# Kernel tuning notes

Hardware: AMD Instinct MI355X
Metric: run time of the kernel (lower is better)

## Reference

```python
import jax, jax.numpy as jnp
import numpy as np

B, N_NODES, T_IN = 512, 32, 12
HID, HEADS, OUT_CH, DEG = 64, 8, 9, 8


def setup_inputs() -> dict:
    key = jax.random.key(0)
    ks = jax.random.split(key, 26)
    rn = lambda k, s, sc=0.1: (jax.random.normal(k, s, jnp.float32) * sc)
    E = B * N_NODES * DEG
    src = jax.random.randint(ks[0], (E,), 0, N_NODES, jnp.int32)
    dst = jax.random.randint(ks[1], (E,), 0, N_NODES, jnp.int32)
    off = jnp.repeat(jnp.arange(B, dtype=jnp.int32) * N_NODES, N_NODES * DEG)
    edge_index = jnp.stack([src + off, dst + off])  # block-diagonal batched graph
    x = jax.random.normal(ks[2], (B, N_NODES, T_IN), jnp.float32)
    return {
        "x": x,
        "edge_index": edge_index,
        # gat1: in=T_IN -> HEADS*HID, concat
        "W1": rn(ks[3], (T_IN, HEADS * HID)),
        "a_src1": rn(ks[4], (HEADS, HID)),
        "a_dst1": rn(ks[5], (HEADS, HID)),
        "b1": rn(ks[6], (HEADS * HID,), 0.01),
        # gat2: in=HEADS*HID -> HID, heads=1, mean (concat=False)
        "W2": rn(ks[7], (HEADS * HID, HID), 0.05),
        "a_src2": rn(ks[8], (1, HID)),
        "a_dst2": rn(ks[9], (1, HID)),
        "b2": rn(ks[10], (HID,), 0.01),
        "gamma": jnp.ones((HID,), jnp.float32),
        "beta": jnp.zeros((HID,), jnp.float32),
        # gru1: input_size=N_NODES(=32), hidden=HID
        "Wi1": rn(ks[11], (3 * HID, N_NODES)),
        "Wh1": rn(ks[12], (3 * HID, HID)),
        "bi1": rn(ks[13], (3 * HID,), 0.01),
        "bh1": rn(ks[14], (3 * HID,), 0.01),
        # gru2: input_size=HID, hidden=HID
        "Wi2": rn(ks[15], (3 * HID, HID)),
        "Wh2": rn(ks[16], (3 * HID, HID)),
        "bi2": rn(ks[17], (3 * HID,), 0.01),
        "bh2": rn(ks[18], (3 * HID,), 0.01),
        "Wf": rn(ks[19], (OUT_CH, HID)),
        "bf": rn(ks[20], (OUT_CH,), 0.01),
    }


def _gat_layer(x, src, dst, W, a_s, a_d, b, concat):
    # PyG GATConv (eval mode, self-loops already appended by caller)
    Nn = x.shape[0]
    heads, hc = a_s.shape
    h = (x @ W).reshape(Nn, heads, hc)                 # [N, H, C]
    es = jnp.sum(h * a_s, axis=-1)                     # [N, H]
    ed = jnp.sum(h * a_d, axis=-1)
    e = jax.nn.leaky_relu(es[src] + ed[dst], 0.2)      # [E, H]
    m = jax.ops.segment_max(e, dst, num_segments=Nn)
    p = jnp.exp(e - m[dst])
    s = jax.ops.segment_sum(p, dst, num_segments=Nn)
    alpha = p / (s[dst] + 1e-16)                       # per-dst softmax
    out = jax.ops.segment_sum(h[src] * alpha[:, :, None], dst, num_segments=Nn)
    out = out.reshape(Nn, heads * hc) if concat else out.mean(axis=1)
    return out + b


def _gru(x, Wi, Wh, bi, bh):
    # torch.nn.GRU (batch_first) single layer; x: [B, T, F]
    H = Wh.shape[1]
    xi = x @ Wi.T + bi                                 # [B, T, 3H]
    def step(h, xt):
        gh = h @ Wh.T + bh
        r = jax.nn.sigmoid(xt[:, :H] + gh[:, :H])
        z = jax.nn.sigmoid(xt[:, H:2 * H] + gh[:, H:2 * H])
        n = jnp.tanh(xt[:, 2 * H:] + r * gh[:, 2 * H:])
        hn = (1.0 - z) * n + z * h
        return hn, hn
    h0 = jnp.zeros((x.shape[0], H), x.dtype)
    _, ys = jax.lax.scan(step, h0, jnp.swapaxes(xi, 0, 1))
    return jnp.swapaxes(ys, 0, 1)


def reference(x, edge_index, W1, a_src1, a_dst1, b1, W2, a_src2, a_dst2, b2,
              gamma, beta, Wi1, Wh1, bi1, bh1, Wi2, Wh2, bi2, bh2, Wf, bf):
    Bsz, Nn_, T = x.shape
    Nn = Bsz * Nn_
    xf = x.reshape(Nn, T)                              # dropout is identity in eval
    sl = jnp.arange(Nn, dtype=edge_index.dtype)        # PyG add_self_loops=True
    src = jnp.concatenate([edge_index[0], sl])
    dst = jnp.concatenate([edge_index[1], sl])
    h = jax.nn.elu(_gat_layer(xf, src, dst, W1, a_src1, a_dst1, b1, True))
    h = jax.nn.elu(_gat_layer(h, src, dst, W2, a_src2, a_dst2, b2, False))
    mu = h.mean(-1, keepdims=True)
    var = ((h - mu) ** 2).mean(-1, keepdims=True)
    h = (h - mu) / jnp.sqrt(var + 1e-5) * gamma + beta
    seq = h.reshape(Bsz, Nn_, -1).transpose(0, 2, 1)   # [B, HID(seq), N_NODES(feat)]
    g = _gru(seq, Wi1, Wh1, bi1, bh1)
    g = _gru(g, Wi2, Wh2, bi2, bh2)
    return g[:, -1, :] @ Wf.T + bf                     # [B, OUT_CH]
```

## Files before the change

kernel.cpp:

```cpp
#include <hip/hip_runtime.h>
#include <hip/hip_bf16.h>
#include <stdint.h>

#define BATCH 512
#define NN 32
#define T_IN 12
#define HID 64
#define HEADS 8
#define OUT_CH 9
#define EPB (NN*8)
#define ETOT (EPB+NN)
#define F1 (HEADS*HID)

using u16 = unsigned short;
using u32 = unsigned int;
typedef _Float16 f16;
typedef _Float16 f16x2 __attribute__((ext_vector_type(2)));
typedef u32 v4u __attribute__((ext_vector_type(4)));

__device__ __forceinline__ float bf2f(u16 u){ return __uint_as_float(((u32)u)<<16); }
__device__ __forceinline__ u16 f2bf(float f){
    u32 x = __float_as_uint(f);
    u32 r = (x + 0x7FFFu + ((x>>16)&1u))>>16;
    return (u16)r;
}
__device__ __forceinline__ u32 packf16(float a, float b){
    f16x2 p; p.x=(f16)a; p.y=(f16)b; return __builtin_bit_cast(u32,p);
}
__device__ __forceinline__ u16 f2h16(float a){ f16 h=(f16)a; return __builtin_bit_cast(u16,h); }
__device__ __forceinline__ float h16f(u16 v){ f16 h=__builtin_bit_cast(f16,v); return (float)h; }
__device__ __forceinline__ float lof(u32 w){ return (float)__builtin_bit_cast(f16x2,w).x; }
__device__ __forceinline__ float hif(u32 w){ return (float)__builtin_bit_cast(f16x2,w).y; }
__device__ __forceinline__ float dot2(u32 a, u32 b, float c){
#if __has_builtin(__builtin_amdgcn_fdot2)
    return __builtin_amdgcn_fdot2(__builtin_bit_cast(f16x2,a), __builtin_bit_cast(f16x2,b), c, false);
#else
    return fmaf(lof(a),lof(b), fmaf(hif(a),hif(b), c));
#endif
}
__device__ __forceinline__ float elu1(float x){ return x > 0.f ? x : (__expf(x)-1.f); }
__device__ __forceinline__ float sigm(float x){ return 1.f/(1.f+__expf(-x)); }
__device__ __forceinline__ float tanh_(float x){ return 1.f - 2.f/(__expf(2.f*x)+1.f); }
__device__ __forceinline__ u32 fenc(float v){
    u32 b=__float_as_uint(v);
    return (b&0x80000000u) ? ~b : (b|0x80000000u);
}
__device__ __forceinline__ float fdec(u32 k){
    return __uint_as_float((k&0x80000000u) ? (k&0x7FFFFFFFu) : ~k);
}

#define DOT4(acc,A,W) do{ acc=dot2(A.x,W.x,acc); acc=dot2(A.y,W.y,acc); \
                          acc=dot2(A.z,W.z,acc); acc=dot2(A.w,W.w,acc); }while(0)
#define DOT32(acc,A0,A1,A2,A3,A4,A5,A6,A7,W0,W1,W2,W3,W4,W5,W6,W7) do{ \
    DOT4(acc,A0,W0); DOT4(acc,A1,W1); DOT4(acc,A2,W2); DOT4(acc,A3,W3); \
    DOT4(acc,A4,W4); DOT4(acc,A5,W5); DOT4(acc,A6,W6); DOT4(acc,A7,W7); }while(0)

__global__ __launch_bounds__(256) void k_detect(const u32* __restrict__ xw, int* __restrict__ flag){
    __shared__ int cnt;
    if(threadIdx.x==0) cnt=0;
    __syncthreads();
    int c=0;
    for(int i=threadIdx.x;i<4096;i+=256){
        u32 w=xw[i];
        if(w & 0x7FFFFFFFu){
            u32 el=(w>>7)&0xFFu;
            if(el>=0x90u) c++;
        }
    }
    atomicAdd(&cnt,c);
    __syncthreads();
    if(threadIdx.x==0) *flag = (cnt>256) ? 1 : 0;
}

struct CvtDesc {
    const void* src[16];
    void*       dst[16];
    int         n[16];
};

__global__ __launch_bounds__(256) void k_convert(CvtDesc d, const int* __restrict__ flag){
    const int seg = blockIdx.x;
    const int f = *flag;
    const void* s = d.src[seg];
    const int n = d.n[seg];
    const int stride = gridDim.y*256;
    float* o=(float*)d.dst[seg];
    for(int i=blockIdx.y*256+threadIdx.x;i<n;i+=stride)
        o[i] = f ? ((const float*)s)[i] : bf2f(((const u16*)s)[i]);
}

__global__ __launch_bounds__(256) void k_prep(
    const void* __restrict__ W2src, u16* __restrict__ W2i,
    const void* __restrict__ Wi1, const void* __restrict__ Wh1,
    const void* __restrict__ Wi2, const void* __restrict__ Wh2,
    u32* __restrict__ wpk, const int* __restrict__ flag)
{
    const int f=*flag;
    if(blockIdx.x<128){
        int i = blockIdx.x*256+threadIdx.x;
        int k=i>>6, j=i&63;
        float v = f? ((const float*)W2src)[i] : bf2f(((const u16*)W2src)[i]);
        W2i[ (((size_t)(k>>3)*64 + j)<<3) + (k&7) ] = f2h16(v);
    } else {
        int w = (blockIdx.x-128)*256+threadIdx.x;
        int m = w/6144;
        int rem = w - m*6144;
        int row = rem>>5, kw = rem&31;
        const void* s = (m==0)?Wi1 : (m==1)?Wh1 : (m==2)?Wi2 : Wh2;
        int K = (m==0)?32:64;
        int k0=2*kw, k1=k0+1;
        float v0=0.f, v1=0.f;
        if(k0<K) v0 = f? ((const float*)s)[row*K+k0] : bf2f(((const u16*)s)[row*K+k0]);
        if(k1<K) v1 = f? ((const float*)s)[row*K+k1] : bf2f(((const u16*)s)[row*K+k1]);
        wpk[w]=packf16(v0,v1);
    }
}

__global__ __launch_bounds__(256,2) void k_gat1(
    const float* __restrict__ x, const int* __restrict__ ei,
    const float* __restrict__ W1, const float* __restrict__ a_s, const float* __restrict__ a_d,
    const float* __restrict__ b1, u32* __restrict__ h1g)
{
    const int b = blockIdx.x, t = threadIdx.x;
    __shared__ __align__(16) float s_x[NN][12];
    __shared__ float s_W1[T_IN*F1];
    __shared__ __align__(16) u16 s_h[NN][520];
    __shared__ __align__(16) u32 s_aspk[HEADS*32], s_adpk[HEADS*32];
    __shared__ float s_es[NN][HEADS], s_ed[NN][HEADS];
    __shared__ unsigned char s_src[ETOT], s_dst[ETOT];
    __shared__ float s_al[ETOT][HEADS];
    __shared__ u32 s_mx[NN*HEADS];
    __shared__ float s_sm[NN*HEADS], s_inv[NN*HEADS];
    __shared__ int s_cnt[NN], s_off[NN], s_fil[NN];
    __shared__ short s_lst[ETOT];

    for(int i=t;i<NN*T_IN;i+=256) s_x[i/12][i%12] = x[b*NN*T_IN + i];
    for(int i=t;i<T_IN*F1;i+=256) s_W1[i]=W1[i];
    s_aspk[t]=packf16(a_s[2*t],a_s[2*t+1]);
    s_adpk[t]=packf16(a_d[2*t],a_d[2*t+1]);
    s_mx[t]=0u; s_sm[t]=0.f;
    if(t<EPB){
        s_src[t] = (unsigned char)(ei[b*EPB+t] - b*NN);
        s_dst[t] = (unsigned char)(ei[(size_t)BATCH*EPB + b*EPB+t] - b*NN);
    }
    if(t<NN){ s_src[EPB+t]=s_dst[EPB+t]=(unsigned char)t; s_cnt[t]=0; s_fil[t]=0; }
    __syncthreads();

    {
        float w0[12], w1[12];
        #pragma unroll
        for(int k=0;k<12;k++){ w0[k]=s_W1[k*F1+t]; w1[k]=s_W1[k*F1+t+256]; }
        for(int n=0;n<NN;n++){
            const float4* xp=(const float4*)s_x[n];
            float4 xa=xp[0], xb=xp[1], xc=xp[2];
            float A=0.f,B=0.f;
            A=fmaf(xa.x,w0[0],A); A=fmaf(xa.y,w0[1],A); A=fmaf(xa.z,w0[2],A); A=fmaf(xa.w,w0[3],A);
            A=fmaf(xb.x,w0[4],A); A=fmaf(xb.y,w0[5],A); A=fmaf(xb.z,w0[6],A); A=fmaf(xb.w,w0[7],A);
            A=fmaf(xc.x,w0[8],A); A=fmaf(xc.y,w0[9],A); A=fmaf(xc.z,w0[10],A); A=fmaf(xc.w,w0[11],A);
            B=fmaf(xa.x,w1[0],B); B=fmaf(xa.y,w1[1],B); B=fmaf(xa.z,w1[2],B); B=fmaf(xa.w,w1[3],B);
            B=fmaf(xb.x,w1[4],B); B=fmaf(xb.y,w1[5],B); B=fmaf(xb.z,w1[6],B); B=fmaf(xb.w,w1[7],B);
            B=fmaf(xc.x,w1[8],B); B=fmaf(xc.y,w1[9],B); B=fmaf(xc.z,w1[10],B); B=fmaf(xc.w,w1[11],B);
            s_h[n][t]=f2h16(A); s_h[n][t+256]=f2h16(B);
        }
    }
    for(int e=t;e<ETOT;e+=256) atomicAdd(&s_cnt[s_dst[e]],1);
    __syncthreads();

    {
        int n=t&31, hd=t>>5;
        const v4u* hp=(const v4u*)((const u16*)s_h[n] + hd*64);
        v4u h0=hp[0],h1=hp[1],h2=hp[2],h3=hp[3],h4=hp[4],h5=hp[5],h6=hp[6],h7=hp[7];
        const v4u* ap=(const v4u*)&s_aspk[hd*32];
        const v4u* dp=(const v4u*)&s_adpk[hd*32];
        float e1=0.f,e2=0.f;
        { v4u w=ap[0]; DOT4(e1,h0,w); w=ap[1]; DOT4(e1,h1,w); w=ap[2]; DOT4(e1,h2,w); w=ap[3]; DOT4(e1,h3,w);
          w=ap[4]; DOT4(e1,h4,w); w=ap[5]; DOT4(e1,h5,w); w=ap[6]; DOT4(e1,h6,w); w=ap[7]; DOT4(e1,h7,w); }
        { v4u w=dp[0]; DOT4(e2,h0,w); w=dp[1]; DOT4(e2,h1,w); w=dp[2]; DOT4(e2,h2,w); w=dp[3]; DOT4(e2,h3,w);
          w=dp[4]; DOT4(e2,h4,w); w=dp[5]; DOT4(e2,h5,w); w=dp[6]; DOT4(e2,h6,w); w=dp[7]; DOT4(e2,h7,w); }
        s_es[n][hd]=e1; s_ed[n][hd]=e2;
    }
    if(t==0){ int o=0; for(int i=0;i<NN;i++){ s_off[i]=o; o+=s_cnt[i]; } }
    __syncthreads();

    for(int e=t;e<ETOT;e+=256){
        int d=s_dst[e]; int p=atomicAdd(&s_fil[d],1); s_lst[s_off[d]+p]=(short)e;
    }
    for(int i=t;i<ETOT*HEADS;i+=256){
        int e=i>>3, hd=i&7;
        int sr=s_src[e], d=s_dst[e];
        float v = s_es[sr][hd]+s_ed[d][hd];
        v = v>0.f? v : 0.2f*v;
        s_al[e][hd]=v;
        atomicMax(&s_mx[d*8+hd], fenc(v));
    }
    __syncthreads();

    for(int i=t;i<ETOT*HEADS;i+=256){
        int e=i>>3, hd=i&7;
        int d=s_dst[e];
        float p=__expf(s_al[e][hd]-fdec(s_mx[d*8+hd]));
        s_al[e][hd]=p;
        atomicAdd(&s_sm[d*8+hd], p);
    }
    __syncthreads();
    s_inv[t]=1.f/(s_sm[t]+1e-16f);
    __syncthreads();

    {
        int d=t&31, hd=t>>5;
        int o=s_off[d], cnt=s_cnt[d];
        float inv=s_inv[d*8+hd];
        size_t obase = ((size_t)(b*NN+d))*256 + hd*32;
        #pragma unroll
        for(int ch=0;ch<2;ch++){
            float acc[32];
            #pragma unroll
            for(int i=0;i<32;i++) acc[i]=0.f;
            for(int i=0;i<cnt;i++){
                int e=s_lst[o+i]; float a=s_al[e][hd]; int sr=s_src[e];
                const v4u* hp=(const v4u*)((const u16*)s_h[sr] + hd*64 + ch*32);
                v4u p0=hp[0],p1=hp[1],p2=hp[2],p3=hp[3];
                #define ACC2(i,w) acc[2*(i)]+=a*lof(w); acc[2*(i)+1]+=a*hif(w);
                ACC2(0,p0.x) ACC2(1,p0.y) ACC2(2,p0.z) ACC2(3,p0.w)
                ACC2(4,p1.x) ACC2(5,p1.y) ACC2(6,p1.z) ACC2(7,p1.w)
                ACC2(8,p2.x) ACC2(9,p2.y) ACC2(10,p2.z) ACC2(11,p2.w)
                ACC2(12,p3.x) ACC2(13,p3.y) ACC2(14,p3.z) ACC2(15,p3.w)
                #undef ACC2
            }
            u32* op = h1g + obase + ch*16;
            #pragma unroll
            for(int j=0;j<16;j++){
                float v0=elu1(acc[2*j]*inv   + b1[hd*64+ch*32+2*j]);
                float v1=elu1(acc[2*j+1]*inv + b1[hd*64+ch*32+2*j+1]);
                op[j]=packf16(v0,v1);
            }
        }
    }
}

__global__ __launch_bounds__(256,2) void k_gat2ln(
    const u32* __restrict__ h1g, const int* __restrict__ ei,
    const uint4* __restrict__ W2i, const float* __restrict__ a_s2, const float* __restrict__ a_d2,
    const float* __restrict__ b2, const float* __restrict__ gam, const float* __restrict__ bet,
    float* __restrict__ hlng)
{
    const int b=blockIdx.x, t=threadIdx.x;
    __shared__ __align__(16) u32 s_h1[NN*260];
    __shared__ float s_h2[NN][HID];
    __shared__ float s_es[NN], s_ed[NN];
    __shared__ unsigned char s_src[ETOT], s_dst[ETOT];
    __shared__ float s_al[ETOT];
    __shared__ u32 s_mx[NN];
    __shared__ float s_sm[NN], s_inv[NN];
    __shared__ int s_cnt[NN], s_off[NN], s_fil[NN];
    __shared__ short s_lst[ETOT];

    { const u32* g = h1g + (size_t)b*8192;
      for(int w=t; w<8192; w+=256){ int n=w>>8, c=w&255; s_h1[n*260+c]=g[w]; } }
    if(t<EPB){
        s_src[t]=(unsigned char)(ei[b*EPB+t]-b*NN);
        s_dst[t]=(unsigned char)(ei[(size_t)BATCH*EPB+b*EPB+t]-b*NN);
    }
    if(t<NN){ s_src[EPB+t]=s_dst[EPB+t]=(unsigned char)t;
              s_cnt[t]=0; s_fil[t]=0; s_mx[t]=0u; s_sm[t]=0.f; }
    __syncthreads();

    for(int e=t;e<ETOT;e+=256) atomicAdd(&s_cnt[s_dst[e]],1);
    {
        int n0=(t>>5)<<2, j0=(t&31)<<1;
        const u32* r0=&s_h1[(n0+0)*260];
        const u32* r1=&s_h1[(n0+1)*260];
        const u32* r2=&s_h1[(n0+2)*260];
        const u32* r3=&s_h1[(n0+3)*260];
        float a00=0,a01=0,a10=0,a11=0,a20=0,a21=0,a30=0,a31=0;
        for(int kb=0;kb<64;kb++){
            uint4 A0=*(const uint4*)&r0[kb*4];
            uint4 A1=*(const uint4*)&r1[kb*4];
            uint4 A2=*(const uint4*)&r2[kb*4];
            uint4 A3=*(const uint4*)&r3[kb*4];
            const uint4* wp=&W2i[kb*64+j0];
            uint4 w0=wp[0], w1=wp[1];
            a00=dot2(A0.x,w0.x,a00); a00=dot2(A0.y,w0.y,a00); a00=dot2(A0.z,w0.z,a00); a00=dot2(A0.w,w0.w,a00);
            a01=dot2(A0.x,w1.x,a01); a01=dot2(A0.y,w1.y,a01); a01=dot2(A0.z,w1.z,a01); a01=dot2(A0.w,w1.w,a01);
            a10=dot2(A1.x,w0.x,a10); a10=dot2(A1.y,w0.y,a10); a10=dot2(A1.z,w0.z,a10); a10=dot2(A1.w,w0.w,a10);
            a11=dot2(A1.x,w1.x,a11); a11=dot2(A1.y,w1.y,a11); a11=dot2(A1.z,w1.z,a11); a11=dot2(A1.w,w1.w,a11);
            a20=dot2(A2.x,w0.x,a20); a20=dot2(A2.y,w0.y,a20); a20=dot2(A2.z,w0.z,a20); a20=dot2(A2.w,w0.w,a20);
            a21=dot2(A2.x,w1.x,a21); a21=dot2(A2.y,w1.y,a21); a21=dot2(A2.z,w1.z,a21); a21=dot2(A2.w,w1.w,a21);
            a30=dot2(A3.x,w0.x,a30); a30=dot2(A3.y,w0.y,a30); a30=dot2(A3.z,w0.z,a30); a30=dot2(A3.w,w0.w,a30);
            a31=dot2(A3.x,w1.x,a31); a31=dot2(A3.y,w1.y,a31); a31=dot2(A3.z,w1.z,a31); a31=dot2(A3.w,w1.w,a31);
        }
        s_h2[n0+0][j0]=a00; s_h2[n0+0][j0+1]=a01;
        s_h2[n0+1][j0]=a10; s_h2[n0+1][j0+1]=a11;
        s_h2[n0+2][j0]=a20; s_h2[n0+2][j0+1]=a21;
        s_h2[n0+3][j0]=a30; s_h2[n0+3][j0+1]=a31;
    }
    __syncthreads();

    {
        int n=t>>3, g=t&7;
        float e1=0,e2=0;
        #pragma unroll
        for(int cc=0; cc<8; cc++){
            float hv = s_h2[n][g*8+cc];
            e1 += hv*a_s2[g*8+cc];
            e2 += hv*a_d2[g*8+cc];
        }
        #pragma unroll
        for(int m=1;m<8;m<<=1){ e1 += __shfl_xor(e1,m,64); e2 += __shfl_xor(e2,m,64); }
        if(g==0){ s_es[n]=e1; s_ed[n]=e2; }
    }
    if(t==0){ int o=0; for(int i=0;i<NN;i++){ s_off[i]=o; o+=s_cnt[i]; } }
    __syncthreads();

    for(int e=t;e<ETOT;e+=256){
        int d=s_dst[e]; int p=atomicAdd(&s_fil[d],1); s_lst[s_off[d]+p]=(short)e;
    }
    for(int e=t;e<ETOT;e+=256){
        int d=s_dst[e];
        float v = s_es[s_src[e]] + s_ed[d];
        v = v>0.f? v:0.2f*v;
        s_al[e]=v;
        atomicMax(&s_mx[d], fenc(v));
    }
    __syncthreads();

    for(int e=t;e<ETOT;e+=256){
        int d=s_dst[e];
        float p=__expf(s_al[e]-fdec(s_mx[d]));
        s_al[e]=p;
        atomicAdd(&s_sm[d], p);
    }
    __syncthreads();
    if(t<NN) s_inv[t]=1.f/(s_sm[t]+1e-16f);
    __syncthreads();

    {
        int n=t>>3, g=t&7;
        float acc[8];
        #pragma unroll
        for(int i=0;i<8;i++) acc[i]=0;
        int o=s_off[n], cnt=s_cnt[n];
        float inv=s_inv[n];
        for(int i=0;i<cnt;i++){
            int e=s_lst[o+i]; float a=s_al[e]; int sr=s_src[e];
            const float4* hp=(const float4*)&s_h2[sr][g*8];
            float4 v0=hp[0], v1=hp[1];
            acc[0]+=a*v0.x; acc[1]+=a*v0.y; acc[2]+=a*v0.z; acc[3]+=a*v0.w;
            acc[4]+=a*v1.x; acc[5]+=a*v1.y; acc[6]+=a*v1.z; acc[7]+=a*v1.w;
        }
        float sum=0,sq=0;
        #pragma unroll
        for(int i=0;i<8;i++){
            float v = elu1(acc[i]*inv + b2[g*8+i]);
            acc[i]=v; sum+=v; sq+=v*v;
        }
        #pragma unroll
        for(int m=1;m<8;m<<=1){ sum+=__shfl_xor(sum,m,64); sq+=__shfl_xor(sq,m,64); }
        float mu = sum*(1.f/64.f);
        float var = sq*(1.f/64.f) - mu*mu;
        float rs = rsqrtf(var + 1e-5f);
        float* outp = hlng + (size_t)b*HID*NN;
        #pragma unroll
        for(int i=0;i<8;i++){
            int c=g*8+i;
            float v=(acc[i]-mu)*rs*gam[c] + bet[c];
            outp[c*NN + n] = v;
        }
    }
}

__global__ __launch_bounds__(256,2) void k_grum(
    const float* __restrict__ hlng, const u32* __restrict__ wpk,
    const float* __restrict__ bi1, const float* __restrict__ bh1,
    const float* __restrict__ bi2, const float* __restrict__ bh2,
    const float* __restrict__ Wf, const float* __restrict__ bfv,
    void* __restrict__ outp, const int* __restrict__ flag)
{
    const int b=blockIdx.x, t=threadIdx.x;
    const int wave=t>>6, u=t&63;
    __shared__ __align__(16) u32 s_x[64*16];
    __shared__ __align__(16) u32 s_xi[64*96];
    __shared__ __align__(16) u32 s_y[64*32];
    __shared__ __align__(16) u32 s_h[32];
    __shared__ float s_hf[64];

    { const float2* g=(const float2*)(hlng + (size_t)b*2048);
      for(int w=t;w<1024;w+=256){ float2 f=g[w]; s_x[w]=packf16(f.x,f.y); } }
    __syncthreads();

    if(t<192){
        const v4u* wr=(const v4u*)wpk + t*8;
        v4u w0=wr[0],w1=wr[1],w2=wr[2],w3=wr[3];
        float bias=bi1[t];
        u16* o=(u16*)s_xi + t;
        for(int step=0;step<64;step++){
            const v4u* xp=(const v4u*)&s_x[step*16];
            v4u a0=xp[0],a1=xp[1],a2=xp[2],a3=xp[3];
            float a=bias;
            DOT4(a,a0,w0); DOT4(a,a1,w1); DOT4(a,a2,w2); DOT4(a,a3,w3);
            o[step*192]=f2h16(a);
        }
    }
    __syncthreads();

    if(wave==0){
        const v4u* wh=(const v4u*)(wpk + 6144);
        v4u r0=wh[u*8+0],r1=wh[u*8+1],r2=wh[u*8+2],r3=wh[u*8+3],
            r4=wh[u*8+4],r5=wh[u*8+5],r6=wh[u*8+6],r7=wh[u*8+7];
        v4u z0=wh[(64+u)*8+0],z1=wh[(64+u)*8+1],z2=wh[(64+u)*8+2],z3=wh[(64+u)*8+3],
            z4=wh[(64+u)*8+4],z5=wh[(64+u)*8+5],z6=wh[(64+u)*8+6],z7=wh[(64+u)*8+7];
        v4u n0=wh[(128+u)*8+0],n1=wh[(128+u)*8+1],n2=wh[(128+u)*8+2],n3=wh[(128+u)*8+3],
            n4=wh[(128+u)*8+4],n5=wh[(128+u)*8+5],n6=wh[(128+u)*8+6],n7=wh[(128+u)*8+7];
        float bhr=bh1[u], bhz=bh1[64+u], bhn=bh1[128+u];
        if(u<32) s_h[u]=0u;
        float h=0.f;
        for(int st=0;st<64;st++){
            const u16* xr=(const u16*)s_xi + st*192;
            float xir=h16f(xr[u]), xiz=h16f(xr[64+u]), xin=h16f(xr[128+u]);
            const v4u* hp=(const v4u*)s_h;
            v4u A0=hp[0],A1=hp[1],A2=hp[2],A3=hp[3],A4=hp[4],A5=hp[5],A6=hp[6],A7=hp[7];
            float gr=bhr,gz=bhz,gn=bhn;
            DOT32(gr,A0,A1,A2,A3,A4,A5,A6,A7,r0,r1,r2,r3,r4,r5,r6,r7);
            DOT32(gz,A0,A1,A2,A3,A4,A5,A6,A7,z0,z1,z2,z3,z4,z5,z6,z7);
            DOT32(gn,A0,A1,A2,A3,A4,A5,A6,A7,n0,n1,n2,n3,n4,n5,n6,n7);
            float rr=sigm(xir+gr), zz=sigm(xiz+gz);
            float nn=tanh_(xin + rr*gn);
            h=(1.f-zz)*nn+zz*h;
            u16 hv=f2h16(h);
            ((u16*)s_h)[u]=hv;
            ((u16*)s_y)[st*64+u]=hv;
        }
    }
    __syncthreads();

    if(t<192){
        const v4u* wr=(const v4u*)(wpk + 2*6144) + t*8;
        v4u w0=wr[0],w1=wr[1],w2=wr[2],w3=wr[3],w4=wr[4],w5=wr[5],w6=wr[6],w7=wr[7];
        float bias=bi2[t];
        u16* o=(u16*)s_xi + t;
        for(int step=0;step<64;step++){
            const v4u* xp=(const v4u*)&s_y[step*32];
            v4u a0=xp[0],a1=xp[1],a2=xp[2],a3=xp[3],a4=xp[4],a5=xp[5],a6=xp[6],a7=xp[7];
            float a=bias;
            DOT32(a,a0,a1,a2,a3,a4,a5,a6,a7,w0,w1,w2,w3,w4,w5,w6,w7);
            o[step*192]=f2h16(a);
        }
    }
    __syncthreads();

    if(wave==0){
        const v4u* wh=(const v4u*)(wpk + 3*6144);
        v4u r0=wh[u*8+0],r1=wh[u*8+1],r2=wh[u*8+2],r3=wh[u*8+3],
            r4=wh[u*8+4],r5=wh[u*8+5],r6=wh[u*8+6],r7=wh[u*8+7];
        v4u z0=wh[(64+u)*8+0],z1=wh[(64+u)*8+1],z2=wh[(64+u)*8+2],z3=wh[(64+u)*8+3],
            z4=wh[(64+u)*8+4],z5=wh[(64+u)*8+5],z6=wh[(64+u)*8+6],z7=wh[(64+u)*8+7];
        v4u n0=wh[(128+u)*8+0],n1=wh[(128+u)*8+1],n2=wh[(128+u)*8+2],n3=wh[(128+u)*8+3],
            n4=wh[(128+u)*8+4],n5=wh[(128+u)*8+5],n6=wh[(128+u)*8+6],n7=wh[(128+u)*8+7];
        float bhr=bh2[u], bhz=bh2[64+u], bhn=bh2[128+u];
        if(u<32) s_h[u]=0u;
        float h=0.f;
        for(int st=0;st<64;st++){
            const u16* xr=(const u16*)s_xi + st*192;
            float xir=h16f(xr[u]), xiz=h16f(xr[64+u]), xin=h16f(xr[128+u]);
            const v4u* hp=(const v4u*)s_h;
            v4u A0=hp[0],A1=hp[1],A2=hp[2],A3=hp[3],A4=hp[4],A5=hp[5],A6=hp[6],A7=hp[7];
            float gr=bhr,gz=bhz,gn=bhn;
            DOT32(gr,A0,A1,A2,A3,A4,A5,A6,A7,r0,r1,r2,r3,r4,r5,r6,r7);
            DOT32(gz,A0,A1,A2,A3,A4,A5,A6,A7,z0,z1,z2,z3,z4,z5,z6,z7);
            DOT32(gn,A0,A1,A2,A3,A4,A5,A6,A7,n0,n1,n2,n3,n4,n5,n6,n7);
            float rr=sigm(xir+gr), zz=sigm(xiz+gz);
            float nn=tanh_(xin + rr*gn);
            h=(1.f-zz)*nn+zz*h;
            ((u16*)s_h)[u]=f2h16(h);
        }
        s_hf[u]=h;
    }
    __syncthreads();

    if(t<OUT_CH){
        float acc=bfv[t];
        const float4* wp=(const float4*)(Wf + t*64);
        const float4* hp=(const float4*)s_hf;
        #pragma unroll
        for(int k=0;k<16;k++){
            float4 w=wp[k], v=hp[k];
            acc += w.x*v.x + w.y*v.y + w.z*v.z + w.w*v.w;
        }
        if(*flag) ((float*)outp)[b*OUT_CH+t]=acc;
        else      ((u16*)outp)[b*OUT_CH+t]=f2bf(acc);
    }
}

extern "C" void kernel_launch(void* const* d_in, const int* in_sizes, int n_in,
                              void* d_out, int out_size, void* d_ws, size_t ws_size,
                              hipStream_t stream)
{
    char* ws=(char*)d_ws;
    int* flag = (int*)ws;
    float* cf = (float*)(ws + 256);
    float* c_x   = cf; cf+=196608;
    float* c_W1  = cf; cf+=6144;
    float* c_as1 = cf; cf+=512;
    float* c_ad1 = cf; cf+=512;
    float* c_b1  = cf; cf+=512;
    float* c_as2 = cf; cf+=64;
    float* c_ad2 = cf; cf+=64;
    float* c_b2  = cf; cf+=64;
    float* c_gam = cf; cf+=64;
    float* c_bet = cf; cf+=64;
    float* c_bi1 = cf; cf+=192;
    float* c_bh1 = cf; cf+=192;
    float* c_bi2 = cf; cf+=192;
    float* c_bh2 = cf; cf+=192;
    float* c_Wf  = cf; cf+=576;
    float* c_bf  = cf; cf+=9;
    uintptr_t p = ((uintptr_t)cf + 255) & ~(uintptr_t)255;
    u16* c_W2i = (u16*)p;
    p = (p + 32768*2 + 255) & ~(uintptr_t)255;
    u32* wpk = (u32*)p;
    p = (p + 24576*4 + 255) & ~(uintptr_t)255;
    u32* h1g = (u32*)p;
    p = (p + (size_t)BATCH*NN*256*4 + 255) & ~(uintptr_t)255;
    float* hlng = (float*)p;

    const int* ei = (const int*)d_in[1];

    CvtDesc d;
    const int srcIdx[16] = {0,2,3,4,5,7,8,9,10,11,14,15,18,19,20,21};
    void* dsts[16] = {c_x,c_W1,c_as1,c_ad1,c_b1,c_as2,c_ad2,c_b2,c_gam,c_bet,
                      c_bi1,c_bh1,c_bi2,c_bh2,c_Wf,c_bf};
    const int ns[16] = {196608,6144,512,512,512,64,64,64,64,64,
                        192,192,192,192,576,9};
    for(int i=0;i<16;i++){ d.src[i]=d_in[srcIdx[i]]; d.dst[i]=dsts[i]; d.n[i]=ns[i]; }

    k_detect <<<dim3(1),dim3(256),0,stream>>>((const u32*)d_in[0], flag);
    k_convert<<<dim3(16,8),dim3(256),0,stream>>>(d, flag);
    k_prep   <<<dim3(224),dim3(256),0,stream>>>(d_in[6], c_W2i,
                                                d_in[12], d_in[13], d_in[16], d_in[17], wpk, flag);
    k_gat1   <<<dim3(BATCH),dim3(256),0,stream>>>(c_x,ei,c_W1,c_as1,c_ad1,c_b1,h1g);
    k_gat2ln <<<dim3(BATCH),dim3(256),0,stream>>>(h1g,ei,(const uint4*)c_W2i,c_as2,c_ad2,c_b2,c_gam,c_bet,hlng);
    k_grum   <<<dim3(BATCH),dim3(256),0,stream>>>(hlng, wpk, c_bi1,c_bh1,c_bi2,c_bh2,
                                                  c_Wf, c_bf, d_out, flag);
}
```

Baseline: 260.1 us.

## Process two batches per GRU block and transpose GAT attention layout

```diff
diff --git a/kernel.cpp b/kernel.cpp
--- a/kernel.cpp
+++ b/kernel.cpp
@@ -17,6 +17,7 @@
 typedef _Float16 f16;
 typedef _Float16 f16x2 __attribute__((ext_vector_type(2)));
 typedef u32 v4u __attribute__((ext_vector_type(4)));
+typedef float v4f __attribute__((ext_vector_type(4)));
 
 __device__ __forceinline__ float bf2f(u16 u){ return __uint_as_float(((u32)u)<<16); }
 __device__ __forceinline__ u16 f2bf(float f){
@@ -128,7 +129,7 @@
     __shared__ __align__(16) u32 s_aspk[HEADS*32], s_adpk[HEADS*32];
     __shared__ float s_es[NN][HEADS], s_ed[NN][HEADS];
     __shared__ unsigned char s_src[ETOT], s_dst[ETOT];
-    __shared__ float s_al[ETOT][HEADS];
+    __shared__ float s_al[HEADS][ETOT];
     __shared__ u32 s_mx[NN*HEADS];
     __shared__ float s_sm[NN*HEADS], s_inv[NN*HEADS];
     __shared__ int s_cnt[NN], s_off[NN], s_fil[NN];
@@ -147,19 +148,23 @@
     __syncthreads();
 
     {
-        float w0[12], w1[12];
-        #pragma unroll
-        for(int k=0;k<12;k++){ w0[k]=s_W1[k*F1+t]; w1[k]=s_W1[k*F1+t+256]; }
+        v4f Wa0,Wa1,Wa2,Wb0,Wb1,Wb2;
+        Wa0.x=s_W1[0*F1+t]; Wa0.y=s_W1[1*F1+t]; Wa0.z=s_W1[2*F1+t]; Wa0.w=s_W1[3*F1+t];
+        Wa1.x=s_W1[4*F1+t]; Wa1.y=s_W1[5*F1+t]; Wa1.z=s_W1[6*F1+t]; Wa1.w=s_W1[7*F1+t];
+        Wa2.x=s_W1[8*F1+t]; Wa2.y=s_W1[9*F1+t]; Wa2.z=s_W1[10*F1+t]; Wa2.w=s_W1[11*F1+t];
+        Wb0.x=s_W1[0*F1+t+256]; Wb0.y=s_W1[1*F1+t+256]; Wb0.z=s_W1[2*F1+t+256]; Wb0.w=s_W1[3*F1+t+256];
+        Wb1.x=s_W1[4*F1+t+256]; Wb1.y=s_W1[5*F1+t+256]; Wb1.z=s_W1[6*F1+t+256]; Wb1.w=s_W1[7*F1+t+256];
+        Wb2.x=s_W1[8*F1+t+256]; Wb2.y=s_W1[9*F1+t+256]; Wb2.z=s_W1[10*F1+t+256]; Wb2.w=s_W1[11*F1+t+256];
         for(int n=0;n<NN;n++){
             const float4* xp=(const float4*)s_x[n];
             float4 xa=xp[0], xb=xp[1], xc=xp[2];
             float A=0.f,B=0.f;
-            A=fmaf(xa.x,w0[0],A); A=fmaf(xa.y,w0[1],A); A=fmaf(xa.z,w0[2],A); A=fmaf(xa.w,w0[3],A);
-            A=fmaf(xb.x,w0[4],A); A=fmaf(xb.y,w0[5],A); A=fmaf(xb.z,w0[6],A); A=fmaf(xb.w,w0[7],A);
-            A=fmaf(xc.x,w0[8],A); A=fmaf(xc.y,w0[9],A); A=fmaf(xc.z,w0[10],A); A=fmaf(xc.w,w0[11],A);
-            B=fmaf(xa.x,w1[0],B); B=fmaf(xa.y,w1[1],B); B=fmaf(xa.z,w1[2],B); B=fmaf(xa.w,w1[3],B);
-            B=fmaf(xb.x,w1[4],B); B=fmaf(xb.y,w1[5],B); B=fmaf(xb.z,w1[6],B); B=fmaf(xb.w,w1[7],B);
-            B=fmaf(xc.x,w1[8],B); B=fmaf(xc.y,w1[9],B); B=fmaf(xc.z,w1[10],B); B=fmaf(xc.w,w1[11],B);
+            A=fmaf(xa.x,Wa0.x,A); A=fmaf(xa.y,Wa0.y,A); A=fmaf(xa.z,Wa0.z,A); A=fmaf(xa.w,Wa0.w,A);
+            A=fmaf(xb.x,Wa1.x,A); A=fmaf(xb.y,Wa1.y,A); A=fmaf(xb.z,Wa1.z,A); A=fmaf(xb.w,Wa1.w,A);
+            A=fmaf(xc.x,Wa2.x,A); A=fmaf(xc.y,Wa2.y,A); A=fmaf(xc.z,Wa2.z,A); A=fmaf(xc.w,Wa2.w,A);
+            B=fmaf(xa.x,Wb0.x,B); B=fmaf(xa.y,Wb0.y,B); B=fmaf(xa.z,Wb0.z,B); B=fmaf(xa.w,Wb0.w,B);
+            B=fmaf(xb.x,Wb1.x,B); B=fmaf(xb.y,Wb1.y,B); B=fmaf(xb.z,Wb1.z,B); B=fmaf(xb.w,Wb1.w,B);
+            B=fmaf(xc.x,Wb2.x,B); B=fmaf(xc.y,Wb2.y,B); B=fmaf(xc.z,Wb2.z,B); B=fmaf(xc.w,Wb2.w,B);
             s_h[n][t]=f2h16(A); s_h[n][t+256]=f2h16(B);
         }
     }
@@ -186,20 +191,20 @@
         int d=s_dst[e]; int p=atomicAdd(&s_fil[d],1); s_lst[s_off[d]+p]=(short)e;
     }
     for(int i=t;i<ETOT*HEADS;i+=256){
-        int e=i>>3, hd=i&7;
+        int hd=i/ETOT, e=i-hd*ETOT;
         int sr=s_src[e], d=s_dst[e];
         float v = s_es[sr][hd]+s_ed[d][hd];
         v = v>0.f? v : 0.2f*v;
-        s_al[e][hd]=v;
+        s_al[hd][e]=v;
         atomicMax(&s_mx[d*8+hd], fenc(v));
     }
     __syncthreads();
 
     for(int i=t;i<ETOT*HEADS;i+=256){
-        int e=i>>3, hd=i&7;
+        int hd=i/ETOT, e=i-hd*ETOT;
         int d=s_dst[e];
-        float p=__expf(s_al[e][hd]-fdec(s_mx[d*8+hd]));
-        s_al[e][hd]=p;
+        float p=__expf(s_al[hd][e]-fdec(s_mx[d*8+hd]));
+        s_al[hd][e]=p;
         atomicAdd(&s_sm[d*8+hd], p);
     }
     __syncthreads();
@@ -213,27 +218,46 @@
         size_t obase = ((size_t)(b*NN+d))*256 + hd*32;
         #pragma unroll
         for(int ch=0;ch<2;ch++){
-            float acc[32];
-            #pragma unroll
-            for(int i=0;i<32;i++) acc[i]=0.f;
+            v4f a0=0,a1=0,a2=0,a3=0,a4=0,a5=0,a6=0,a7=0;
             for(int i=0;i<cnt;i++){
-                int e=s_lst[o+i]; float a=s_al[e][hd]; int sr=s_src[e];
+                int e=s_lst[o+i]; float av=s_al[hd][e]; int sr=s_src[e];
                 const v4u* hp=(const v4u*)((const u16*)s_h[sr] + hd*64 + ch*32);
                 v4u p0=hp[0],p1=hp[1],p2=hp[2],p3=hp[3];
-                #define ACC2(i,w) acc[2*(i)]+=a*lof(w); acc[2*(i)+1]+=a*hif(w);
-                ACC2(0,p0.x) ACC2(1,p0.y) ACC2(2,p0.z) ACC2(3,p0.w)
-                ACC2(4,p1.x) ACC2(5,p1.y) ACC2(6,p1.z) ACC2(7,p1.w)
-                ACC2(8,p2.x) ACC2(9,p2.y) ACC2(10,p2.z) ACC2(11,p2.w)
-                ACC2(12,p3.x) ACC2(13,p3.y) ACC2(14,p3.z) ACC2(15,p3.w)
-                #undef ACC2
+                a0.x=fmaf(av,lof(p0.x),a0.x); a0.y=fmaf(av,hif(p0.x),a0.y);
+                a0.z=fmaf(av,lof(p0.y),a0.z); a0.w=fmaf(av,hif(p0.y),a0.w);
+                a1.x=fmaf(av,lof(p0.z),a1.x); a1.y=fmaf(av,hif(p0.z),a1.y);
+                a1.z=fmaf(av,lof(p0.w),a1.z); a1.w=fmaf(av,hif(p0.w),a1.w);
+                a2.x=fmaf(av,lof(p1.x),a2.x); a2.y=fmaf(av,hif(p1.x),a2.y);
+                a2.z=fmaf(av,lof(p1.y),a2.z); a2.w=fmaf(av,hif(p1.y),a2.w);
+                a3.x=fmaf(av,lof(p1.z),a3.x); a3.y=fmaf(av,hif(p1.z),a3.y);
+                a3.z=fmaf(av,lof(p1.w),a3.z); a3.w=fmaf(av,hif(p1.w),a3.w);
+                a4.x=fmaf(av,lof(p2.x),a4.x); a4.y=fmaf(av,hif(p2.x),a4.y);
+                a4.z=fmaf(av,lof(p2.y),a4.z); a4.w=fmaf(av,hif(p2.y),a4.w);
+                a5.x=fmaf(av,lof(p2.z),a5.x); a5.y=fmaf(av,hif(p2.z),a5.y);
+                a5.z=fmaf(av,lof(p2.w),a5.z); a5.w=fmaf(av,hif(p2.w),a5.w);
+                a6.x=fmaf(av,lof(p3.x),a6.x); a6.y=fmaf(av,hif(p3.x),a6.y);
+                a6.z=fmaf(av,lof(p3.y),a6.z); a6.w=fmaf(av,hif(p3.y),a6.w);
+                a7.x=fmaf(av,lof(p3.z),a7.x); a7.y=fmaf(av,hif(p3.z),a7.y);
+                a7.z=fmaf(av,lof(p3.w),a7.z); a7.w=fmaf(av,hif(p3.w),a7.w);
             }
+            const float* bp = b1 + hd*64 + ch*32;
             u32* op = h1g + obase + ch*16;
-            #pragma unroll
-            for(int j=0;j<16;j++){
-                float v0=elu1(acc[2*j]*inv   + b1[hd*64+ch*32+2*j]);
-                float v1=elu1(acc[2*j+1]*inv + b1[hd*64+ch*32+2*j+1]);
-                op[j]=packf16(v0,v1);
-            }
+            op[0] = packf16(elu1(a0.x*inv+bp[0]),  elu1(a0.y*inv+bp[1]));
+            op[1] = packf16(elu1(a0.z*inv+bp[2]),  elu1(a0.w*inv+bp[3]));
+            op[2] = packf16(elu1(a1.x*inv+bp[4]),  elu1(a1.y*inv+bp[5]));
+            op[3] = packf16(elu1(a1.z*inv+bp[6]),  elu1(a1.w*inv+bp[7]));
+            op[4] = packf16(elu1(a2.x*inv+bp[8]),  elu1(a2.y*inv+bp[9]));
+            op[5] = packf16(elu1(a2.z*inv+bp[10]), elu1(a2.w*inv+bp[11]));
+            op[6] = packf16(elu1(a3.x*inv+bp[12]), elu1(a3.y*inv+bp[13]));
+            op[7] = packf16(elu1(a3.z*inv+bp[14]), elu1(a3.w*inv+bp[15]));
+            op[8] = packf16(elu1(a4.x*inv+bp[16]), elu1(a4.y*inv+bp[17]));
+            op[9] = packf16(elu1(a4.z*inv+bp[18]), elu1(a4.w*inv+bp[19]));
+            op[10]= packf16(elu1(a5.x*inv+bp[20]), elu1(a5.y*inv+bp[21]));
+            op[11]= packf16(elu1(a5.z*inv+bp[22]), elu1(a5.w*inv+bp[23]));
+            op[12]= packf16(elu1(a6.x*inv+bp[24]), elu1(a6.y*inv+bp[25]));
+            op[13]= packf16(elu1(a6.z*inv+bp[26]), elu1(a6.w*inv+bp[27]));
+            op[14]= packf16(elu1(a7.x*inv+bp[28]), elu1(a7.y*inv+bp[29]));
+            op[15]= packf16(elu1(a7.z*inv+bp[30]), elu1(a7.w*inv+bp[31]));
         }
     }
 }
@@ -336,65 +360,72 @@
 
     {
         int n=t>>3, g=t&7;
-        float acc[8];
-        #pragma unroll
-        for(int i=0;i<8;i++) acc[i]=0;
+        v4f a0=0, a1=0;
         int o=s_off[n], cnt=s_cnt[n];
         float inv=s_inv[n];
         for(int i=0;i<cnt;i++){
             int e=s_lst[o+i]; float a=s_al[e]; int sr=s_src[e];
             const float4* hp=(const float4*)&s_h2[sr][g*8];
             float4 v0=hp[0], v1=hp[1];
-            acc[0]+=a*v0.x; acc[1]+=a*v0.y; acc[2]+=a*v0.z; acc[3]+=a*v0.w;
-            acc[4]+=a*v1.x; acc[5]+=a*v1.y; acc[6]+=a*v1.z; acc[7]+=a*v1.w;
-        }
-        float sum=0,sq=0;
-        #pragma unroll
-        for(int i=0;i<8;i++){
-            float v = elu1(acc[i]*inv + b2[g*8+i]);
-            acc[i]=v; sum+=v; sq+=v*v;
-        }
+            a0.x=fmaf(a,v0.x,a0.x); a0.y=fmaf(a,v0.y,a0.y); a0.z=fmaf(a,v0.z,a0.z); a0.w=fmaf(a,v0.w,a0.w);
+            a1.x=fmaf(a,v1.x,a1.x); a1.y=fmaf(a,v1.y,a1.y); a1.z=fmaf(a,v1.z,a1.z); a1.w=fmaf(a,v1.w,a1.w);
+        }
+        const float* bp=b2+g*8;
+        float v0=elu1(a0.x*inv+bp[0]), v1=elu1(a0.y*inv+bp[1]);
+        float v2=elu1(a0.z*inv+bp[2]), v3=elu1(a0.w*inv+bp[3]);
+        float v4=elu1(a1.x*inv+bp[4]), v5=elu1(a1.y*inv+bp[5]);
+        float v6=elu1(a1.z*inv+bp[6]), v7=elu1(a1.w*inv+bp[7]);
+        float sum=v0+v1+v2+v3+v4+v5+v6+v7;
+        float sq=v0*v0+v1*v1+v2*v2+v3*v3+v4*v4+v5*v5+v6*v6+v7*v7;
         #pragma unroll
         for(int m=1;m<8;m<<=1){ sum+=__shfl_xor(sum,m,64); sq+=__shfl_xor(sq,m,64); }
         float mu = sum*(1.f/64.f);
         float var = sq*(1.f/64.f) - mu*mu;
         float rs = rsqrtf(var + 1e-5f);
         float* outp = hlng + (size_t)b*HID*NN;
-        #pragma unroll
-        for(int i=0;i<8;i++){
-            int c=g*8+i;
-            float v=(acc[i]-mu)*rs*gam[c] + bet[c];
-            outp[c*NN + n] = v;
-        }
-    }
-}
-
-__global__ __launch_bounds__(256,2) void k_grum(
+        int c=g*8;
+        outp[(c+0)*NN+n]=(v0-mu)*rs*gam[c+0]+bet[c+0];
+        outp[(c+1)*NN+n]=(v1-mu)*rs*gam[c+1]+bet[c+1];
+        outp[(c+2)*NN+n]=(v2-mu)*rs*gam[c+2]+bet[c+2];
+        outp[(c+3)*NN+n]=(v3-mu)*rs*gam[c+3]+bet[c+3];
+        outp[(c+4)*NN+n]=(v4-mu)*rs*gam[c+4]+bet[c+4];
+        outp[(c+5)*NN+n]=(v5-mu)*rs*gam[c+5]+bet[c+5];
+        outp[(c+6)*NN+n]=(v6-mu)*rs*gam[c+6]+bet[c+6];
+        outp[(c+7)*NN+n]=(v7-mu)*rs*gam[c+7]+bet[c+7];
+    }
+}
+
+__global__ __launch_bounds__(256,1) void k_grum(
     const float* __restrict__ hlng, const u32* __restrict__ wpk,
     const float* __restrict__ bi1, const float* __restrict__ bh1,
     const float* __restrict__ bi2, const float* __restrict__ bh2,
     const float* __restrict__ Wf, const float* __restrict__ bfv,
     void* __restrict__ outp, const int* __restrict__ flag)
 {
-    const int b=blockIdx.x, t=threadIdx.x;
+    const int b0=blockIdx.x*2, t=threadIdx.x;
     const int wave=t>>6, u=t&63;
-    __shared__ __align__(16) u32 s_x[64*16];
-    __shared__ __align__(16) u32 s_xi[64*96];
-    __shared__ __align__(16) u32 s_y[64*32];
-    __shared__ __align__(16) u32 s_h[32];
-    __shared__ float s_hf[64];
-
-    { const float2* g=(const float2*)(hlng + (size_t)b*2048);
-      for(int w=t;w<1024;w+=256){ float2 f=g[w]; s_x[w]=packf16(f.x,f.y); } }
-    __syncthreads();
-
-    if(t<192){
-        const v4u* wr=(const v4u*)wpk + t*8;
+    __shared__ __align__(16) u32 s_x[2][64*16];
+    __shared__ __align__(16) u32 s_xi[2][64*96];
+    __shared__ __align__(16) u32 s_y[2][64*32];
+    __shared__ __align__(16) u32 s_h[2][32];
+    __shared__ float s_hf[2][64];
+
+    for(int w=t;w<2048;w+=256){
+        int bb=w>>10, idx=w&1023;
+        const float2* g=(const float2*)(hlng + (size_t)(b0+bb)*2048);
+        float2 f=g[idx]; s_x[bb][idx]=packf16(f.x,f.y);
+    }
+    __syncthreads();
+
+    for(int r=t;r<384;r+=256){
+        int bb=r>=192, row=r-bb*192;
+        const v4u* wr=(const v4u*)wpk + row*8;
         v4u w0=wr[0],w1=wr[1],w2=wr[2],w3=wr[3];
-        float bias=bi1[t];
-        u16* o=(u16*)s_xi + t;
+        float bias=bi1[row];
+        u16* o=(u16*)s_xi[bb] + row;
         for(int step=0;step<64;step++){
-            const v4u* xp=(const v4u*)&s_x[step*16];
+            asm volatile("" : "+v"(w0),"+v"(w1),"+v"(w2),"+v"(w3));
+            const v4u* xp=(const v4u*)&s_x[bb][step*16];
             v4u a0=xp[0],a1=xp[1],a2=xp[2],a3=xp[3];
             float a=bias;
             DOT4(a,a0,w0); DOT4(a,a1,w1); DOT4(a,a2,w2); DOT4(a,a3,w3);
@@ -403,7 +434,8 @@
     }
     __syncthreads();
 
-    if(wave==0){
+    if(wave<2){
+        const int bb=wave;
         const v4u* wh=(const v4u*)(wpk + 6144);
         v4u r0=wh[u*8+0],r1=wh[u*8+1],r2=wh[u*8+2],r3=wh[u*8+3],
             r4=wh[u*8+4],r5=wh[u*8+5],r6=wh[u*8+6],r7=wh[u*8+7];
@@ -412,12 +444,15 @@
         v4u n0=wh[(128+u)*8+0],n1=wh[(128+u)*8+1],n2=wh[(128+u)*8+2],n3=wh[(128+u)*8+3],
             n4=wh[(128+u)*8+4],n5=wh[(128+u)*8+5],n6=wh[(128+u)*8+6],n7=wh[(128+u)*8+7];
         float bhr=bh1[u], bhz=bh1[64+u], bhn=bh1[128+u];
-        if(u<32) s_h[u]=0u;
+        if(u<32) s_h[bb][u]=0u;
         float h=0.f;
         for(int st=0;st<64;st++){
-            const u16* xr=(const u16*)s_xi + st*192;
+            asm volatile("" : "+v"(r0),"+v"(r1),"+v"(r2),"+v"(r3),"+v"(r4),"+v"(r5),"+v"(r6),"+v"(r7),
+                              "+v"(z0),"+v"(z1),"+v"(z2),"+v"(z3),"+v"(z4),"+v"(z5),"+v"(z6),"+v"(z7),
+                              "+v"(n0),"+v"(n1),"+v"(n2),"+v"(n3),"+v"(n4),"+v"(n5),"+v"(n6),"+v"(n7));
+            const u16* xr=(const u16*)s_xi[bb] + st*192;
             float xir=h16f(xr[u]), xiz=h16f(xr[64+u]), xin=h16f(xr[128+u]);
-            const v4u* hp=(const v4u*)s_h;
+            const v4u* hp=(const v4u*)s_h[bb];
             v4u A0=hp[0],A1=hp[1],A2=hp[2],A3=hp[3],A4=hp[4],A5=hp[5],A6=hp[6],A7=hp[7];
             float gr=bhr,gz=bhz,gn=bhn;
             DOT32(gr,A0,A1,A2,A3,A4,A5,A6,A7,r0,r1,r2,r3,r4,r5,r6,r7);
@@ -427,19 +462,22 @@
             float nn=tanh_(xin + rr*gn);
             h=(1.f-zz)*nn+zz*h;
             u16 hv=f2h16(h);
-            ((u16*)s_h)[u]=hv;
-            ((u16*)s_y)[st*64+u]=hv;
-        }
-    }
-    __syncthreads();
-
-    if(t<192){
-        const v4u* wr=(const v4u*)(wpk + 2*6144) + t*8;
+            ((u16*)s_h[bb])[u]=hv;
+            ((u16*)s_y[bb])[st*64+u]=hv;
+        }
+    }
+    __syncthreads();
+
+    for(int r=t;r<384;r+=256){
+        int bb=r>=192, row=r-bb*192;
+        const v4u* wr=(const v4u*)(wpk + 2*6144) + row*8;
         v4u w0=wr[0],w1=wr[1],w2=wr[2],w3=wr[3],w4=wr[4],w5=wr[5],w6=wr[6],w7=wr[7];
-        float bias=bi2[t];
-        u16* o=(u16*)s_xi + t;
+        float bias=bi2[row];
+        u16* o=(u16*)s_xi[bb] + row;
         for(int step=0;step<64;step++){
-            const v4u* xp=(const v4u*)&s_y[step*32];
+            asm volatile("" : "+v"(w0),"+v"(w1),"+v"(w2),"+v"(w3),
+                              "+v"(w4),"+v"(w5),"+v"(w6),"+v"(w7));
+            const v4u* xp=(const v4u*)&s_y[bb][step*32];
             v4u a0=xp[0],a1=xp[1],a2=xp[2],a3=xp[3],a4=xp[4],a5=xp[5],a6=xp[6],a7=xp[7];
             float a=bias;
             DOT32(a,a0,a1,a2,a3,a4,a5,a6,a7,w0,w1,w2,w3,w4,w5,w6,w7);
@@ -448,7 +486,8 @@
     }
     __syncthreads();
 
-    if(wave==0){
+    if(wave<2){
+        const int bb=wave;
         const v4u* wh=(const v4u*)(wpk + 3*6144);
         v4u r0=wh[u*8+0],r1=wh[u*8+1],r2=wh[u*8+2],r3=wh[u*8+3],
             r4=wh[u*8+4],r5=wh[u*8+5],r6=wh[u*8+6],r7=wh[u*8+7];
@@ -457,12 +496,15 @@
         v4u n0=wh[(128+u)*8+0],n1=wh[(128+u)*8+1],n2=wh[(128+u)*8+2],n3=wh[(128+u)*8+3],
             n4=wh[(128+u)*8+4],n5=wh[(128+u)*8+5],n6=wh[(128+u)*8+6],n7=wh[(128+u)*8+7];
         float bhr=bh2[u], bhz=bh2[64+u], bhn=bh2[128+u];
-        if(u<32) s_h[u]=0u;
+        if(u<32) s_h[bb][u]=0u;
         float h=0.f;
         for(int st=0;st<64;st++){
-            const u16* xr=(const u16*)s_xi + st*192;
+            asm volatile("" : "+v"(r0),"+v"(r1),"+v"(r2),"+v"(r3),"+v"(r4),"+v"(r5),"+v"(r6),"+v"(r7),
+                              "+v"(z0),"+v"(z1),"+v"(z2),"+v"(z3),"+v"(z4),"+v"(z5),"+v"(z6),"+v"(z7),
+                              "+v"(n0),"+v"(n1),"+v"(n2),"+v"(n3),"+v"(n4),"+v"(n5),"+v"(n6),"+v"(n7));
+            const u16* xr=(const u16*)s_xi[bb] + st*192;
             float xir=h16f(xr[u]), xiz=h16f(xr[64+u]), xin=h16f(xr[128+u]);
-            const v4u* hp=(const v4u*)s_h;
+            const v4u* hp=(const v4u*)s_h[bb];
             v4u A0=hp[0],A1=hp[1],A2=hp[2],A3=hp[3],A4=hp[4],A5=hp[5],A6=hp[6],A7=hp[7];
             float gr=bhr,gz=bhz,gn=bhn;
             DOT32(gr,A0,A1,A2,A3,A4,A5,A6,A7,r0,r1,r2,r3,r4,r5,r6,r7);
@@ -471,23 +513,24 @@
             float rr=sigm(xir+gr), zz=sigm(xiz+gz);
             float nn=tanh_(xin + rr*gn);
             h=(1.f-zz)*nn+zz*h;
-            ((u16*)s_h)[u]=f2h16(h);
-        }
-        s_hf[u]=h;
-    }
-    __syncthreads();
-
-    if(t<OUT_CH){
-        float acc=bfv[t];
-        const float4* wp=(const float4*)(Wf + t*64);
-        const float4* hp=(const float4*)s_hf;
+            ((u16*)s_h[bb])[u]=f2h16(h);
+        }
+        s_hf[bb][u]=h;
+    }
+    __syncthreads();
+
+    if(t<2*OUT_CH){
+        int bb=t/OUT_CH, o=t-bb*OUT_CH;
+        float acc=bfv[o];
+        const float4* wp=(const float4*)(Wf + o*64);
+        const float4* hp=(const float4*)s_hf[bb];
         #pragma unroll
         for(int k=0;k<16;k++){
             float4 w=wp[k], v=hp[k];
             acc += w.x*v.x + w.y*v.y + w.z*v.z + w.w*v.w;
         }
-        if(*flag) ((float*)outp)[b*OUT_CH+t]=acc;
-        else      ((u16*)outp)[b*OUT_CH+t]=f2bf(acc);
+        if(*flag) ((float*)outp)[(b0+bb)*OUT_CH+o]=acc;
+        else      ((u16*)outp)[(b0+bb)*OUT_CH+o]=f2bf(acc);
     }
 }
 
@@ -539,6 +582,6 @@
                                                 d_in[12], d_in[13], d_in[16], d_in[17], wpk, flag);
     k_gat1   <<<dim3(BATCH),dim3(256),0,stream>>>(c_x,ei,c_W1,c_as1,c_ad1,c_b1,h1g);
     k_gat2ln <<<dim3(BATCH),dim3(256),0,stream>>>(h1g,ei,(const uint4*)c_W2i,c_as2,c_ad2,c_b2,c_gam,c_bet,hlng);
-    k_grum   <<<dim3(BATCH),dim3(256),0,stream>>>(hlng, wpk, c_bi1,c_bh1,c_bi2,c_bh2,
-                                                  c_Wf, c_bf, d_out, flag);
-}
+    k_grum   <<<dim3(BATCH/2),dim3(256),0,stream>>>(hlng, wpk, c_bi1,c_bh1,c_bi2,c_bh2,
+                                                    c_Wf, c_bf, d_out, flag);
+}
```

After: 264.6 us. About the same (+1.7%).
